# Performance work log

Hardware: AMD Instinct MI355X
Metric: run time of the kernel (lower is better)

## Reference

```python
import jax, jax.numpy as jnp
import numpy as np

# camera / raster constants
N = 10000            # gaussians
W = 256
H = 256
FX = 200.0
FY = 200.0
TILE = 16
NTX = W // TILE
NTY = H // TILE
NT = NTX * NTY       # 256 tiles
P = TILE * TILE      # 256 pixels per tile
K = 256              # max gaussians kept per tile
NEAR = 0.3
MAGIC = 1.2          # frustum expansion factor from project_culling
LP = 0.3 / (FX * FX) # low-pass filter added to 2D covariance diagonal


def quat_to_rot(q):
    w, x, y, z = q[:, 0], q[:, 1], q[:, 2], q[:, 3]
    r0 = jnp.stack([1 - 2 * (y * y + z * z), 2 * (x * y - w * z), 2 * (x * z + w * y)], -1)
    r1 = jnp.stack([2 * (x * y + w * z), 1 - 2 * (x * x + z * z), 2 * (y * z - w * x)], -1)
    r2 = jnp.stack([2 * (x * z - w * y), 2 * (y * z + w * x), 1 - 2 * (x * x + y * y)], -1)
    return jnp.stack([r0, r1, r2], axis=1)  # [N,3,3]


def splat_forward(pos, rgb, opacity, quaternion, scale, w2c_r, w2c_t):
    # ---- project + frustum cull (global_culling) ----
    q = quaternion / jnp.linalg.norm(quaternion, axis=-1, keepdims=True)
    R = quat_to_rot(q)
    sigma = jnp.exp(scale)                               # normalize_scale
    cov3d = jnp.einsum('nij,nj,nkj->nik', R, sigma * sigma, R)
    p_cam = pos @ w2c_r.T + w2c_t                        # [N,3]
    x, y, z = p_cam[:, 0], p_cam[:, 1], p_cam[:, 2]
    zc = jnp.maximum(z, 1e-6)
    half_w = W * MAGIC / 2 / FX
    half_h = H * MAGIC / 2 / FY
    mean2d = jnp.stack([x / zc, y / zc], -1)             # camera-plane coords
    in_frustum = (z > NEAR) & (jnp.abs(mean2d[:, 0]) < half_w) & (jnp.abs(mean2d[:, 1]) < half_h)
    iz = 1.0 / zc
    zero = jnp.zeros_like(iz)
    J = jnp.stack([jnp.stack([iz, zero, -x * iz * iz], -1),
                   jnp.stack([zero, iz, -y * iz * iz], -1)], axis=1)  # [N,2,3]
    cov_cam = jnp.einsum('ij,njk,lk->nil', w2c_r, cov3d, w2c_r)
    cov2d = jnp.einsum('nij,njk,nlk->nil', J, cov_cam, J)            # [N,2,2]
    a = cov2d[:, 0, 0] + LP
    c = cov2d[:, 1, 1] + LP
    b = cov2d[:, 0, 1]

    # ---- per-tile culling + fixed-K binning (calc_tile_list / gather_gaussians) ----
    cx = (jnp.arange(NTX) * TILE + TILE / 2 - W / 2) / FX
    cy = (jnp.arange(NTY) * TILE + TILE / 2 - H / 2) / FY
    centers = jnp.stack(jnp.meshgrid(cx, cy, indexing='xy'), -1).reshape(NT, 2)  # [NT,2] (ty-major)
    tile_half_diag = 0.5 * jnp.sqrt((TILE / FX) ** 2 + (TILE / FY) ** 2)
    mid = 0.5 * (a + c)
    sigma_max = jnp.sqrt(jnp.maximum(mid + jnp.sqrt(jnp.maximum((0.5 * (a - c)) ** 2 + b * b, 0.0)), 1e-12))
    dist = jnp.linalg.norm(centers[:, None, :] - mean2d[None, :, :], axis=-1)   # [NT,N]
    valid = in_frustum[None, :] & (dist <= (3.0 * sigma_max + tile_half_diag)[None, :])
    score = jnp.where(valid, -dist, -1e10)
    vals, idx = jax.lax.top_k(score, K)                                          # [NT,K]
    valid_k = vals > -1e9

    mean_g = mean2d[idx]                     # [NT,K,2]
    z_g = z[idx]
    a_g, b_g, c_g = a[idx], b[idx], c[idx]
    opa_g = jax.nn.sigmoid(opacity)[idx]
    rgb_g = jax.nn.sigmoid(rgb)[idx]         # [NT,K,3]

    # ---- depth sort within each tile ----
    order = jnp.argsort(jnp.where(valid_k, z_g, jnp.inf), axis=-1)
    def srt(arr):
        o = order.reshape(order.shape + (1,) * (arr.ndim - 2))
        return jnp.take_along_axis(arr, o, axis=1)
    mean_s, a_s, b_s, c_s = srt(mean_g), srt(a_g), srt(b_g), srt(c_g)
    opa_s, rgb_s = srt(opa_g), srt(rgb_g)
    valid_s = srt(valid_k).astype(pos.dtype)

    # ---- per-pixel front-to-back alpha compositing (draw) ----
    px = ((jnp.arange(W) + 0.5 - W / 2) / FX).reshape(NTX, TILE)
    py = ((jnp.arange(H) + 0.5 - H / 2) / FY).reshape(NTY, TILE)
    U = jnp.broadcast_to(px[None, :, None, :], (NTY, NTX, TILE, TILE)).reshape(NT, P)
    V = jnp.broadcast_to(py[:, None, :, None], (NTY, NTX, TILE, TILE)).reshape(NT, P)
    dx = U[:, :, None] - mean_s[:, None, :, 0]          # [NT,P,K]
    dy = V[:, :, None] - mean_s[:, None, :, 1]
    det = jnp.maximum(a_s * c_s - b_s * b_s, 1e-12)[:, None, :]
    maha = (c_s[:, None, :] * dx * dx - 2.0 * b_s[:, None, :] * dx * dy + a_s[:, None, :] * dy * dy) / det
    alpha = jnp.clip(opa_s[:, None, :] * jnp.exp(-0.5 * maha), 0.0, 0.99) * valid_s[:, None, :]
    trans = jnp.cumprod(1.0 - alpha, axis=-1)
    texc = jnp.concatenate([jnp.ones_like(trans[..., :1]), trans[..., :-1]], axis=-1)
    color = jnp.einsum('tpk,tkc->tpc', alpha * texc, rgb_s)  # [NT,P,3]
    img = color.reshape(NTY, NTX, TILE, TILE, 3).transpose(0, 2, 1, 3, 4).reshape(H, W, 3)
    return jnp.clip(img, 0.0, 1.0)


def setup_inputs() -> dict:
    key = jax.random.key(0)
    ks = jax.random.split(key, 6)
    zpos = jax.random.uniform(ks[0], (N,), minval=2.0, maxval=6.0)
    uv = jax.random.uniform(ks[1], (N, 2), minval=-0.6, maxval=0.6)
    pos = jnp.concatenate([uv * zpos[:, None], zpos[:, None]], axis=-1)
    rgb = jax.random.normal(ks[2], (N, 3))              # pre-sigmoid logits
    opacity = jax.random.normal(ks[3], (N,)) + 1.5      # sigmoid -> ~0.8 like init_opacity
    quaternion = jax.random.normal(ks[4], (N, 4))
    scale = 0.2 * jax.random.normal(ks[5], (N, 3)) - 4.5  # exp -> ~0.01 world sigma
    w2c_r = jnp.eye(3, dtype=jnp.float32)
    w2c_t = jnp.zeros((3,), dtype=jnp.float32)
    return {"pos": pos, "rgb": rgb, "opacity": opacity, "quaternion": quaternion,
            "scale": scale, "w2c_r": w2c_r, "w2c_t": w2c_t}


def reference(pos, rgb, opacity, quaternion, scale, w2c_r, w2c_t):
    return splat_forward(pos, rgb, opacity, quaternion, scale, w2c_r, w2c_t)
```

## Files before the change

kernel.cpp:

```cpp
#include <hip/hip_runtime.h>
#include <math.h>

namespace {
constexpr int W = 256, H = 256, TILE = 16, NTX = 16, NT = 256, K = 256;
constexpr float FX = 200.0f, FY = 200.0f, NEARP = 0.3f, MAGIC = 1.2f;
constexpr float LP = 0.3f / (FX * FX);
constexpr float HALF_W = W * MAGIC / 2.0f / FX;
constexpr float HALF_H = H * MAGIC / 2.0f / FY;
constexpr float THDIAG = 0.05656854249492381f;
constexpr int CAP = 1024;
constexpr int N_PAD = 10240;
constexpr int BT = 1024;
constexpr int NB_MAX = 64;
constexpr int SEG = 256;
constexpr size_t A_OFF  = 0;
constexpr size_t B_OFF  = A_OFF + (size_t)N_PAD * 16;
constexpr size_t C_OFF  = B_OFF + (size_t)N_PAD * 16;
constexpr size_t SL_OFF = C_OFF + (size_t)N_PAD * 16;
constexpr size_t LD_OFF = SL_OFF + (size_t)NT * NB_MAX * 4;
constexpr size_t LZ_OFF = LD_OFF + (size_t)NT * NB_MAX * SEG * 8;
constexpr size_t WS_FULL = LZ_OFF + (size_t)NT * NB_MAX * SEG * 8;
}

struct Pre { float mx, my, z, a, b, c, radius; };

__device__ inline Pre preprocess(int g, const float* __restrict__ pos,
                                 const float* __restrict__ quat,
                                 const float* __restrict__ scl,
                                 const float* __restrict__ w2cr,
                                 const float* __restrict__ w2ct) {
  float p0 = pos[3*g+0], p1 = pos[3*g+1], p2 = pos[3*g+2];
  float qw = quat[4*g+0], qx = quat[4*g+1], qy = quat[4*g+2], qz = quat[4*g+3];
  float inv = 1.0f / sqrtf(qw*qw + qx*qx + qy*qy + qz*qz);
  qw *= inv; qx *= inv; qy *= inv; qz *= inv;
  float r00 = 1.f-2.f*(qy*qy+qz*qz), r01 = 2.f*(qx*qy-qw*qz), r02 = 2.f*(qx*qz+qw*qy);
  float r10 = 2.f*(qx*qy+qw*qz), r11 = 1.f-2.f*(qx*qx+qz*qz), r12 = 2.f*(qy*qz-qw*qx);
  float r20 = 2.f*(qx*qz-qw*qy), r21 = 2.f*(qy*qz+qw*qx), r22 = 1.f-2.f*(qx*qx+qy*qy);
  float e0 = expf(scl[3*g+0]); float s0 = e0*e0;
  float e1 = expf(scl[3*g+1]); float s1 = e1*e1;
  float e2 = expf(scl[3*g+2]); float s2 = e2*e2;
  float C00 = r00*r00*s0 + r01*r01*s1 + r02*r02*s2;
  float C01 = r00*r10*s0 + r01*r11*s1 + r02*r12*s2;
  float C02 = r00*r20*s0 + r01*r21*s1 + r02*r22*s2;
  float C11 = r10*r10*s0 + r11*r11*s1 + r12*r12*s2;
  float C12 = r10*r20*s0 + r11*r21*s1 + r12*r22*s2;
  float C22 = r20*r20*s0 + r21*r21*s1 + r22*r22*s2;
  float w00=w2cr[0],w01=w2cr[1],w02=w2cr[2];
  float w10=w2cr[3],w11=w2cr[4],w12=w2cr[5];
  float w20=w2cr[6],w21=w2cr[7],w22=w2cr[8];
  float x = w00*p0 + w01*p1 + w02*p2 + w2ct[0];
  float y = w10*p0 + w11*p1 + w12*p2 + w2ct[1];
  float z = w20*p0 + w21*p1 + w22*p2 + w2ct[2];
  float m00 = w00*C00 + w01*C01 + w02*C02;
  float m01 = w00*C01 + w01*C11 + w02*C12;
  float m02 = w00*C02 + w01*C12 + w02*C22;
  float m10 = w10*C00 + w11*C01 + w12*C02;
  float m11 = w10*C01 + w11*C11 + w12*C12;
  float m12 = w10*C02 + w11*C12 + w12*C22;
  float m20 = w20*C00 + w21*C01 + w22*C02;
  float m21 = w20*C01 + w21*C11 + w22*C12;
  float m22 = w20*C02 + w21*C12 + w22*C22;
  float v00 = m00*w00 + m01*w01 + m02*w02;
  float v01 = m00*w10 + m01*w11 + m02*w12;
  float v02 = m00*w20 + m01*w21 + m02*w22;
  float v10 = m10*w00 + m11*w01 + m12*w02;
  float v11 = m10*w10 + m11*w11 + m12*w12;
  float v12 = m10*w20 + m11*w21 + m12*w22;
  float v20 = m20*w00 + m21*w01 + m22*w02;
  float v21 = m20*w10 + m21*w11 + m22*w12;
  float v22 = m20*w20 + m21*w21 + m22*w22;
  float zc = fmaxf(z, 1e-6f);
  float iz = 1.0f / zc;
  float mx = x * iz, my = y * iz;
  float iz2 = iz * iz;
  float jx = -x * iz2, jy = -y * iz2;
  float a00 = iz*v00 + jx*v20, a01 = iz*v01 + jx*v21, a02 = iz*v02 + jx*v22;
  float a10 = iz*v10 + jy*v20, a11 = iz*v11 + jy*v21, a12 = iz*v12 + jy*v22;
  float A  = a00*iz + a02*jx + LP;
  float Bv = a01*iz + a02*jy;
  float Cv = a11*iz + a12*jy + LP;
  float mid = 0.5f*(A + Cv);
  float hh  = 0.5f*(A - Cv);
  float disc = fmaxf(hh*hh + Bv*Bv, 0.0f);
  float smax = sqrtf(fmaxf(mid + sqrtf(disc), 1e-12f));
  bool infr = (z > NEARP) && (fabsf(mx) < HALF_W) && (fabsf(my) < HALF_H);
  Pre r;
  r.mx = mx; r.my = my; r.z = z; r.a = A; r.b = Bv; r.c = Cv;
  r.radius = infr ? (3.0f * smax + THDIAG) : -1.0f;
  return r;
}


template <bool BIN>
__global__ __launch_bounds__(256)
void pre_bin(const float* __restrict__ pos, const float* __restrict__ rgb,
             const float* __restrict__ opac, const float* __restrict__ quat,
             const float* __restrict__ scl, const float* __restrict__ w2cr,
             const float* __restrict__ w2ct,
             float4* __restrict__ pa, float4* __restrict__ pb,
             float4* __restrict__ pc, int* __restrict__ seglen,
             unsigned long long* __restrict__ listd,
             unsigned long long* __restrict__ listz, int n) {
  __shared__ int s_tc[NT];
  const int tid = (int)threadIdx.x;
  const int blk = (int)blockIdx.x;
  if (BIN) {
    if (tid < NT) s_tc[tid] = 0;
    __syncthreads();
  }
  const int g = blk * 256 + tid;
  if (g < n) {
    Pre p = preprocess(g, pos, quat, scl, w2cr, w2ct);
    float det = fmaxf(p.a * p.c - p.b * p.b, 1e-12f);
    float ivd = 1.0f / det;
    float lopa = -__logf(1.0f + __expf(-opac[g]));
    pa[g] = make_float4(p.mx, p.my, p.radius, p.z);
    pb[g] = make_float4(-0.5f * ivd * p.c, ivd * p.b, -0.5f * ivd * p.a, lopa);
    pc[g] = make_float4(1.0f / (1.0f + __expf(-rgb[3*g+0])),
                        1.0f / (1.0f + __expf(-rgb[3*g+1])),
                        1.0f / (1.0f + __expf(-rgb[3*g+2])), 0.0f);
    if (BIN && p.radius >= 0.0f) {
      float r = p.radius;
      int txlo = max(0,     (int)floorf(((p.mx - r) * FX + 120.0f) * 0.0625f));
      int txhi = min(NTX-1, (int)ceilf (((p.mx + r) * FX + 120.0f) * 0.0625f));
      int tylo = max(0,     (int)floorf(((p.my - r) * FY + 120.0f) * 0.0625f));
      int tyhi = min(NTX-1, (int)ceilf (((p.my + r) * FY + 120.0f) * 0.0625f));
      unsigned long long gbits = (unsigned int)g;
      for (int ty = tylo; ty <= tyhi; ++ty) {
        float cy = (ty * TILE + TILE * 0.5f - H * 0.5f) / FY;
        float ddy = cy - p.my;
        for (int tx = txlo; tx <= txhi; ++tx) {
          float cx = (tx * TILE + TILE * 0.5f - W * 0.5f) / FX;
          float ddx = cx - p.mx;
          float dist = sqrtf(ddx * ddx + ddy * ddy);
          if (dist <= r) {
            int t = ty * NTX + tx;
            int slot = atomicAdd(&s_tc[t], 1);
            size_t idx = ((size_t)t * NB_MAX + blk) * SEG + slot;
            listd[idx] = ((unsigned long long)__float_as_uint(dist) << 32) | gbits;
            listz[idx] = ((unsigned long long)__float_as_uint(p.z)  << 32) | gbits;
          }
        }
      }
    }
  }
  if (BIN) {
    __syncthreads();
    if (tid < NT) seglen[(size_t)tid * NB_MAX + blk] = s_tc[tid];
  }
}


__device__ inline void hsort1(unsigned long long* key, int M) {
  const int tid = (int)threadIdx.x;
  __syncthreads();
  unsigned long long e = (tid < M) ? key[tid] : ~0ull;
  for (int k = 2; k <= M; k <<= 1) {
    for (int j = k >> 1; j >= 64; j >>= 1) {
      __syncthreads();
      if (tid < M) key[tid] = e;
      __syncthreads();
      if (tid < M) {
        unsigned long long p = key[tid ^ j];
        bool takeMin = (((tid & j) == 0) == ((tid & k) == 0));
        e = ((p < e) == takeMin) ? p : e;
      }
    }
    int j0 = ((k >> 1) < 32) ? (k >> 1) : 32;
    for (int j = j0; j >= 1; j >>= 1) {
      unsigned long long p = __shfl_xor(e, j, 64);
      bool takeMin = (((tid & j) == 0) == ((tid & k) == 0));
      e = ((p < e) == takeMin) ? p : e;
    }
  }
  __syncthreads();
  if (tid < M) key[tid] = e;
  __syncthreads();
}


__device__ inline void tail8(
    const float4* __restrict__ pa, const float4* __restrict__ pb,
    const float4* __restrict__ pc, float* __restrict__ out,
    unsigned long long* s_zkey, int* s_rank,
    float4* s_p0, float4* s_p1, float* s_cb, float4* s_part,
    int cnt2, int tx, int ty) {
  const int tid = (int)threadIdx.x;
  {
    const int e = tid & 255;
    const int q = tid >> 8;
    if (e < cnt2) {
      unsigned long long mykey = s_zkey[e];
      int jlo = q * 64;
      int jhi = min(cnt2, jlo + 64);
      int partial = 0;
      for (int j = jlo; j < jhi; ++j)
        partial += (s_zkey[j] < mykey) ? 1 : 0;
      if (partial) atomicAdd(&s_rank[e], partial);
    }
  }
  __syncthreads();
  if (tid < cnt2) {
    int g = (int)(s_zkey[tid] & 0xffffffffu);
    int r = s_rank[tid];
    float4 A = pa[g], B = pb[g], C = pc[g];
    s_p0[r] = make_float4(A.x, A.y, B.x, B.y);
    s_p1[r] = make_float4(B.z, B.w, C.x, C.y);
    s_cb[r] = C.z;
  }
  __syncthreads();

  const int p7 = tid & 127;
  const int q8 = tid >> 7;
  const int prl = p7 >> 4;
  const int pcol = p7 & 15;
  const float u   = ((float)(tx * TILE + pcol) + 0.5f - W * 0.5f) / FX;
  const float vlo = ((float)(ty * TILE + prl) + 0.5f - H * 0.5f) / FY;
  const float vhi = ((float)(ty * TILE + prl + 8) + 0.5f - H * 0.5f) / FY;
  const int chunk = (cnt2 + 7) >> 3;
  const int k0 = q8 * chunk;
  const int k1 = min(cnt2, k0 + chunk);
  float Tl = 1.0f, lr = 0.0f, lg = 0.0f, lb = 0.0f;
  float Th = 1.0f, hr = 0.0f, hg = 0.0f, hb = 0.0f;
  for (int k2 = k0; k2 < k1; ++k2) {
    float4 P0 = s_p0[k2];
    float4 P1 = s_p1[k2];
    float cb = s_cb[k2];
    float dx = u - P0.x;
    float s  = fmaf(P0.z * dx, dx, P1.y);
    float bd = P0.w * dx;
    float dyl = vlo - P0.y;
    float ml  = fmaf(fmaf(P1.x, dyl, bd), dyl, s);
    float al  = fminf(__expf(ml), 0.99f);
    float wl  = al * Tl;
    lr = fmaf(wl, P1.z, lr); lg = fmaf(wl, P1.w, lg); lb = fmaf(wl, cb, lb);
    Tl = fmaf(-al, Tl, Tl);
    float dyh = vhi - P0.y;
    float mh  = fmaf(fmaf(P1.x, dyh, bd), dyh, s);
    float ah  = fminf(__expf(mh), 0.99f);
    float wh  = ah * Th;
    hr = fmaf(wh, P1.z, hr); hg = fmaf(wh, P1.w, hg); hb = fmaf(wh, cb, hb);
    Th = fmaf(-ah, Th, Th);
  }
  s_part[q8 * 256 + p7]       = make_float4(lr, lg, lb, Tl);
  s_part[q8 * 256 + 128 + p7] = make_float4(hr, hg, hb, Th);
  __syncthreads();

  if (tid < 256) {
    float4 P = s_part[7 * 256 + tid];
    float r = P.x, g = P.y, b = P.z;
    #pragma unroll
    for (int q = 6; q >= 0; --q) {
      float4 Q = s_part[q * 256 + tid];
      r = fmaf(Q.w, r, Q.x);
      g = fmaf(Q.w, g, Q.y);
      b = fmaf(Q.w, b, Q.z);
    }
    const int prow = tid / TILE, pcol2 = tid % TILE;
    const int row = ty * TILE + prow;
    const int col = tx * TILE + pcol2;
    const int o = (row * W + col) * 3;
    out[o+0] = fminf(fmaxf(r, 0.0f), 1.0f);
    out[o+1] = fminf(fmaxf(g, 0.0f), 1.0f);
    out[o+2] = fminf(fmaxf(b, 0.0f), 1.0f);
  }
}


__global__ __launch_bounds__(BT)
void render_list(const float4* __restrict__ pa, const float4* __restrict__ pb,
                 const float4* __restrict__ pc, const int* __restrict__ seglen,
                 const unsigned long long* __restrict__ listd,
                 const unsigned long long* __restrict__ listz,
                 float* __restrict__ out, int nb) {
  __shared__ unsigned long long s_zkey[CAP];
  __shared__ unsigned long long s_dkey[CAP];
  __shared__ int s_off[NB_MAX + 1];
  __shared__ int s_rank[K];
  __shared__ float4 s_p0[K];
  __shared__ float4 s_p1[K];
  __shared__ float  s_cb[K];
  __shared__ float4 s_part[8 * 256];

  const int t  = (int)blockIdx.x;
  const int tx = t % NTX;
  const int ty = t / NTX;
  const int tid = (int)threadIdx.x;

  if (tid < K) s_rank[tid] = 0;
  if (tid < 64) {
    int v = (tid < nb) ? seglen[(size_t)t * NB_MAX + tid] : 0;
    #pragma unroll
    for (int d = 1; d < 64; d <<= 1) {
      int u2 = __shfl_up(v, d, 64);
      if (tid >= d) v += u2;
    }
    if (tid == 0) s_off[0] = 0;
    if (tid < nb) s_off[tid + 1] = v;
  }
  __syncthreads();
  int cnt = min(s_off[nb], CAP);

  for (int i = tid; i < cnt; i += BT) {
    int lo = 0, hi = nb;
    while (hi - lo > 1) {
      int mid = (lo + hi) >> 1;
      if (s_off[mid] <= i) lo = mid; else hi = mid;
    }
    size_t src = ((size_t)t * NB_MAX + lo) * SEG + (size_t)(i - s_off[lo]);
    s_zkey[i] = listz[src];
  }
  __syncthreads();
  int cnt2 = cnt;

  if (cnt > K) {
    for (int i = tid; i < cnt; i += BT) {
      int lo = 0, hi = nb;
      while (hi - lo > 1) {
        int mid = (lo + hi) >> 1;
        if (s_off[mid] <= i) lo = mid; else hi = mid;
      }
      size_t src = ((size_t)t * NB_MAX + lo) * SEG + (size_t)(i - s_off[lo]);
      s_dkey[i] = listd[src];
    }
    int M = 512; while (M < cnt) M <<= 1;
    for (int i = cnt + tid; i < M; i += BT) s_dkey[i] = ~0ull;
    hsort1(s_dkey, M);
    if (tid < K) {
      int g = (int)(s_dkey[tid] & 0xffffffffu);
      s_zkey[tid] = ((unsigned long long)__float_as_uint(pa[g].w) << 32) |
                    (unsigned int)g;
    }
    __syncthreads();
    cnt2 = K;
  }

  tail8(pa, pb, pc, out, s_zkey, s_rank, s_p0, s_p1, s_cb, s_part, cnt2, tx, ty);
}


__global__ __launch_bounds__(BT)
void render_scan(const float4* __restrict__ pa, const float4* __restrict__ pb,
                 const float4* __restrict__ pc, float* __restrict__ out, int n) {
  __shared__ unsigned long long s_zkey[CAP];
  __shared__ unsigned long long s_dkey[CAP];
  __shared__ int s_rank[K];
  __shared__ float4 s_p0[K];
  __shared__ float4 s_p1[K];
  __shared__ float  s_cb[K];
  __shared__ float4 s_part[8 * 256];
  __shared__ int s_cnt;

  const int t  = (int)blockIdx.x;
  const int tx = t % NTX;
  const int ty = t / NTX;
  const int tid = (int)threadIdx.x;
  const int lane = tid & 63;
  const float cxc = (tx * TILE + TILE * 0.5f - W * 0.5f) / FX;
  const float cyc = (ty * TILE + TILE * 0.5f - H * 0.5f) / FY;

  if (tid == 0) s_cnt = 0;
  if (tid < K) s_rank[tid] = 0;
  __syncthreads();

  for (int g = tid; g < n; g += BT) {
    float4 v = pa[g];
    float ddx = cxc - v.x, ddy = cyc - v.y;
    float dist = sqrtf(ddx * ddx + ddy * ddy);
    bool hit = (v.z >= 0.0f) && (dist <= v.z);
    unsigned long long m = __ballot(hit);
    if (m) {
      int leader = __ffsll((long long)m) - 1;
      int base = 0;
      if (lane == leader) base = atomicAdd(&s_cnt, __popcll(m));
      base = __shfl(base, leader, 64);
      if (hit) {
        int slot = base + __popcll(m & ((1ull << lane) - 1ull));
        if (slot < CAP) {
          s_dkey[slot] = ((unsigned long long)__float_as_uint(dist) << 32) |
                         (unsigned int)g;
          s_zkey[slot] = ((unsigned long long)__float_as_uint(v.w) << 32) |
                         (unsigned int)g;
        }
      }
    }
  }
  __syncthreads();
  int cnt = min(s_cnt, CAP);
  int cnt2 = cnt;

  if (cnt > K) {
    int M = 512; while (M < cnt) M <<= 1;
    for (int i = cnt + tid; i < M; i += BT) s_dkey[i] = ~0ull;
    hsort1(s_dkey, M);
    if (tid < K) {
      int g = (int)(s_dkey[tid] & 0xffffffffu);
      s_zkey[tid] = ((unsigned long long)__float_as_uint(pa[g].w) << 32) |
                    (unsigned int)g;
    }
    __syncthreads();
    cnt2 = K;
  }

  tail8(pa, pb, pc, out, s_zkey, s_rank, s_p0, s_p1, s_cb, s_part, cnt2, tx, ty);
}

extern "C" void kernel_launch(void* const* d_in, const int* in_sizes, int n_in,
                              void* d_out, int out_size, void* d_ws, size_t ws_size,
                              hipStream_t stream) {
  const float* pos  = (const float*)d_in[0];
  const float* rgb  = (const float*)d_in[1];
  const float* opac = (const float*)d_in[2];
  const float* quat = (const float*)d_in[3];
  const float* scl  = (const float*)d_in[4];
  const float* w2cr = (const float*)d_in[5];
  const float* w2ct = (const float*)d_in[6];
  float* out = (float*)d_out;
  const int n = in_sizes[0] / 3;
  const int nb = (n + 255) / 256;

  char* ws = (char*)d_ws;
  float4* pa = (float4*)(ws + A_OFF);
  float4* pb = (float4*)(ws + B_OFF);
  float4* pc = (float4*)(ws + C_OFF);
  int* seglen = (int*)(ws + SL_OFF);
  unsigned long long* listd = (unsigned long long*)(ws + LD_OFF);
  unsigned long long* listz = (unsigned long long*)(ws + LZ_OFF);

  if (ws_size >= WS_FULL && nb <= NB_MAX) {
    pre_bin<true><<<nb, 256, 0, stream>>>(
        pos, rgb, opac, quat, scl, w2cr, w2ct, pa, pb, pc, seglen, listd, listz, n);
    render_list<<<NT, BT, 0, stream>>>(pa, pb, pc, seglen, listd, listz, out, nb);
  } else {
    pre_bin<false><<<nb, 256, 0, stream>>>(
        pos, rgb, opac, quat, scl, w2cr, w2ct, pa, pb, pc, seglen, listd, listz, n);
    render_scan<<<NT, BT, 0, stream>>>(pa, pb, pc, out, n);
  }
}
```

Baseline: 22.26 us.

## Split tile compositing into 16 depth chunks with four pixel rows per thread

The blending stage now splits the sorted gaussian list into 16 depth chunks instead of 8. Each thread handles four pixel rows, sharing the per-gaussian x terms across them, and the partial results are merged in a longer front-to-back combine. The rank-counting loop now uses a chunk size derived from the count rather than a fixed 64, and the scale exponentials switch to fast __expf. This shortens the serial per-thread loop and raises ILP, at the cost of doubling the shared-memory partial buffer (32KB) and a longer merge.

Measured after the change: 21.17 us (median of 2 runs). 1.05x faster.

```diff
diff --git a/kernel.cpp b/kernel.cpp
--- a/kernel.cpp
+++ b/kernel.cpp
@@ -13,6 +13,7 @@
 constexpr int BT = 1024;
 constexpr int NB_MAX = 64;
 constexpr int SEG = 256;
+constexpr int NSPL = 16;
 constexpr size_t A_OFF  = 0;
 constexpr size_t B_OFF  = A_OFF + (size_t)N_PAD * 16;
 constexpr size_t C_OFF  = B_OFF + (size_t)N_PAD * 16;
@@ -36,9 +37,9 @@
   float r00 = 1.f-2.f*(qy*qy+qz*qz), r01 = 2.f*(qx*qy-qw*qz), r02 = 2.f*(qx*qz+qw*qy);
   float r10 = 2.f*(qx*qy+qw*qz), r11 = 1.f-2.f*(qx*qx+qz*qz), r12 = 2.f*(qy*qz-qw*qx);
   float r20 = 2.f*(qx*qz-qw*qy), r21 = 2.f*(qy*qz+qw*qx), r22 = 1.f-2.f*(qx*qx+qy*qy);
-  float e0 = expf(scl[3*g+0]); float s0 = e0*e0;
-  float e1 = expf(scl[3*g+1]); float s1 = e1*e1;
-  float e2 = expf(scl[3*g+2]); float s2 = e2*e2;
+  float e0 = __expf(scl[3*g+0]); float s0 = e0*e0;
+  float e1 = __expf(scl[3*g+1]); float s1 = e1*e1;
+  float e2 = __expf(scl[3*g+2]); float s2 = e2*e2;
   float C00 = r00*r00*s0 + r01*r01*s1 + r02*r02*s2;
   float C01 = r00*r10*s0 + r01*r11*s1 + r02*r12*s2;
   float C02 = r00*r20*s0 + r01*r21*s1 + r02*r22*s2;
@@ -179,7 +180,7 @@
 }
 
 
-__device__ inline void tail8(
+__device__ inline void tail16(
     const float4* __restrict__ pa, const float4* __restrict__ pb,
     const float4* __restrict__ pc, float* __restrict__ out,
     unsigned long long* s_zkey, int* s_rank,
@@ -189,10 +190,11 @@
   {
     const int e = tid & 255;
     const int q = tid >> 8;
+    const int rchunk = (cnt2 + 3) >> 2;
     if (e < cnt2) {
       unsigned long long mykey = s_zkey[e];
-      int jlo = q * 64;
-      int jhi = min(cnt2, jlo + 64);
+      int jlo = q * rchunk;
+      int jhi = min(cnt2, jlo + rchunk);
       int partial = 0;
       for (int j = jlo; j < jhi; ++j)
         partial += (s_zkey[j] < mykey) ? 1 : 0;
@@ -210,18 +212,22 @@
   }
   __syncthreads();
 
-  const int p7 = tid & 127;
-  const int q8 = tid >> 7;
-  const int prl = p7 >> 4;
-  const int pcol = p7 & 15;
-  const float u   = ((float)(tx * TILE + pcol) + 0.5f - W * 0.5f) / FX;
-  const float vlo = ((float)(ty * TILE + prl) + 0.5f - H * 0.5f) / FY;
-  const float vhi = ((float)(ty * TILE + prl + 8) + 0.5f - H * 0.5f) / FY;
-  const int chunk = (cnt2 + 7) >> 3;
-  const int k0 = q8 * chunk;
+  const int p6  = tid & 63;
+  const int q16 = tid >> 6;
+  const int prow0 = p6 >> 4;
+  const int pcol  = p6 & 15;
+  const float u  = ((float)(tx * TILE + pcol) + 0.5f - W * 0.5f) / FX;
+  const float v0 = ((float)(ty * TILE + prow0 +  0) + 0.5f - H * 0.5f) / FY;
+  const float v1 = ((float)(ty * TILE + prow0 +  4) + 0.5f - H * 0.5f) / FY;
+  const float v2 = ((float)(ty * TILE + prow0 +  8) + 0.5f - H * 0.5f) / FY;
+  const float v3 = ((float)(ty * TILE + prow0 + 12) + 0.5f - H * 0.5f) / FY;
+  const int chunk = (cnt2 + NSPL - 1) / NSPL;
+  const int k0 = q16 * chunk;
   const int k1 = min(cnt2, k0 + chunk);
-  float Tl = 1.0f, lr = 0.0f, lg = 0.0f, lb = 0.0f;
-  float Th = 1.0f, hr = 0.0f, hg = 0.0f, hb = 0.0f;
+  float T0 = 1.0f, r0 = 0.0f, g0 = 0.0f, b0 = 0.0f;
+  float T1 = 1.0f, r1 = 0.0f, g1 = 0.0f, b1 = 0.0f;
+  float T2 = 1.0f, r2 = 0.0f, g2 = 0.0f, b2 = 0.0f;
+  float T3 = 1.0f, r3 = 0.0f, g3 = 0.0f, b3 = 0.0f;
   for (int k2 = k0; k2 < k1; ++k2) {
     float4 P0 = s_p0[k2];
     float4 P1 = s_p1[k2];
@@ -229,34 +235,59 @@
     float dx = u - P0.x;
     float s  = fmaf(P0.z * dx, dx, P1.y);
     float bd = P0.w * dx;
-    float dyl = vlo - P0.y;
-    float ml  = fmaf(fmaf(P1.x, dyl, bd), dyl, s);
-    float al  = fminf(__expf(ml), 0.99f);
-    float wl  = al * Tl;
-    lr = fmaf(wl, P1.z, lr); lg = fmaf(wl, P1.w, lg); lb = fmaf(wl, cb, lb);
-    Tl = fmaf(-al, Tl, Tl);
-    float dyh = vhi - P0.y;
-    float mh  = fmaf(fmaf(P1.x, dyh, bd), dyh, s);
-    float ah  = fminf(__expf(mh), 0.99f);
-    float wh  = ah * Th;
-    hr = fmaf(wh, P1.z, hr); hg = fmaf(wh, P1.w, hg); hb = fmaf(wh, cb, hb);
-    Th = fmaf(-ah, Th, Th);
-  }
-  s_part[q8 * 256 + p7]       = make_float4(lr, lg, lb, Tl);
-  s_part[q8 * 256 + 128 + p7] = make_float4(hr, hg, hb, Th);
+    {
+      float dy = v0 - P0.y;
+      float m  = fmaf(fmaf(P1.x, dy, bd), dy, s);
+      float a  = fminf(__expf(m), 0.99f);
+      float w  = a * T0;
+      r0 = fmaf(w, P1.z, r0); g0 = fmaf(w, P1.w, g0); b0 = fmaf(w, cb, b0);
+      T0 = fmaf(-a, T0, T0);
+    }
+    {
+      float dy = v1 - P0.y;
+      float m  = fmaf(fmaf(P1.x, dy, bd), dy, s);
+      float a  = fminf(__expf(m), 0.99f);
+      float w  = a * T1;
+      r1 = fmaf(w, P1.z, r1); g1 = fmaf(w, P1.w, g1); b1 = fmaf(w, cb, b1);
+      T1 = fmaf(-a, T1, T1);
+    }
+    {
+      float dy = v2 - P0.y;
+      float m  = fmaf(fmaf(P1.x, dy, bd), dy, s);
+      float a  = fminf(__expf(m), 0.99f);
+      float w  = a * T2;
+      r2 = fmaf(w, P1.z, r2); g2 = fmaf(w, P1.w, g2); b2 = fmaf(w, cb, b2);
+      T2 = fmaf(-a, T2, T2);
+    }
+    {
+      float dy = v3 - P0.y;
+      float m  = fmaf(fmaf(P1.x, dy, bd), dy, s);
+      float a  = fminf(__expf(m), 0.99f);
+      float w  = a * T3;
+      r3 = fmaf(w, P1.z, r3); g3 = fmaf(w, P1.w, g3); b3 = fmaf(w, cb, b3);
+      T3 = fmaf(-a, T3, T3);
+    }
+  }
+  s_part[q16 * 256 + p6 +   0] = make_float4(r0, g0, b0, T0);
+  s_part[q16 * 256 + p6 +  64] = make_float4(r1, g1, b1, T1);
+  s_part[q16 * 256 + p6 + 128] = make_float4(r2, g2, b2, T2);
+  s_part[q16 * 256 + p6 + 192] = make_float4(r3, g3, b3, T3);
   __syncthreads();
 
   if (tid < 256) {
-    float4 P = s_part[7 * 256 + tid];
+    float4 P = s_part[(NSPL - 1) * 256 + tid];
     float r = P.x, g = P.y, b = P.z;
     #pragma unroll
-    for (int q = 6; q >= 0; --q) {
+    for (int q = NSPL - 2; q >= 0; --q) {
       float4 Q = s_part[q * 256 + tid];
       r = fmaf(Q.w, r, Q.x);
       g = fmaf(Q.w, g, Q.y);
       b = fmaf(Q.w, b, Q.z);
     }
-    const int prow = tid / TILE, pcol2 = tid % TILE;
+    const int p6o = tid & 63;
+    const int sub = tid >> 6;
+    const int prow = (p6o >> 4) + 4 * sub;
+    const int pcol2 = p6o & 15;
     const int row = ty * TILE + prow;
     const int col = tx * TILE + pcol2;
     const int o = (row * W + col) * 3;
@@ -280,7 +311,7 @@
   __shared__ float4 s_p0[K];
   __shared__ float4 s_p1[K];
   __shared__ float  s_cb[K];
-  __shared__ float4 s_part[8 * 256];
+  __shared__ float4 s_part[NSPL * 256];
 
   const int t  = (int)blockIdx.x;
   const int tx = t % NTX;
@@ -335,7 +366,7 @@
     cnt2 = K;
   }
 
-  tail8(pa, pb, pc, out, s_zkey, s_rank, s_p0, s_p1, s_cb, s_part, cnt2, tx, ty);
+  tail16(pa, pb, pc, out, s_zkey, s_rank, s_p0, s_p1, s_cb, s_part, cnt2, tx, ty);
 }
 
 
@@ -348,7 +379,7 @@
   __shared__ float4 s_p0[K];
   __shared__ float4 s_p1[K];
   __shared__ float  s_cb[K];
-  __shared__ float4 s_part[8 * 256];
+  __shared__ float4 s_part[NSPL * 256];
   __shared__ int s_cnt;
 
   const int t  = (int)blockIdx.x;
@@ -402,7 +433,7 @@
     cnt2 = K;
   }
 
-  tail8(pa, pb, pc, out, s_zkey, s_rank, s_p0, s_p1, s_cb, s_part, cnt2, tx, ty);
+  tail16(pa, pb, pc, out, s_zkey, s_rank, s_p0, s_p1, s_cb, s_part, cnt2, tx, ty);
 }
 
 extern "C" void kernel_launch(void* const* d_in, const int* in_sizes, int n_in,
```
